# Optimization experiments

Hardware: AMD Instinct MI355X
Metric: run time of the kernel (lower is better)

## Reference

```python
import jax, jax.numpy as jnp
import numpy as np

B, CIN, H, W = 32, 64, 112, 112
COUT, KH, KW = 64, 3, 3
STRIDE = (1, 1)
PADDING = ((1, 1), (1, 1))
DILATION = (1, 1)


def setup_inputs() -> dict:
    key = jax.random.key(0)
    k1, k2, k3 = jax.random.split(key, 3)
    # quantized activations and weights, int8 value range [-128, 127]
    x_q = jax.random.randint(k1, (B, CIN, H, W), -128, 128, dtype=jnp.int32).astype(jnp.int8)
    w_q = jax.random.randint(k2, (COUT, CIN, KH, KW), -128, 128, dtype=jnp.int32).astype(jnp.int8)
    weight_scale = jnp.float32(0.02)   # per-tensor weight scale
    act_scale = jnp.float32(0.05)      # per-tensor activation scale
    bias = jax.random.normal(k3, (COUT,), dtype=jnp.float32)
    return {"x_q": x_q, "w_q": w_q, "weight_scale": weight_scale,
            "act_scale": act_scale, "bias": bias}


def reference(x_q, w_q, weight_scale, act_scale, bias):
    acc = jax.lax.conv_general_dilated(
        x_q.astype(jnp.int32), w_q.astype(jnp.int32),
        window_strides=STRIDE, padding=PADDING, rhs_dilation=DILATION,
        dimension_numbers=("NCHW", "OIHW", "NCHW"),
        preferred_element_type=jnp.int32)
    # fused dequant (per-tensor scales) + FP32 bias -> FP32 output [B, COUT, H, W]
    out = acc.astype(jnp.float32) * (act_scale * weight_scale) + bias[None, :, None, None]
    return out
```

## Files before the change

### kernel.cpp

```cpp
#include <hip/hip_runtime.h>
#include <stdint.h>

#define BATCH 32
#define CIN   64
#define HH    112
#define WW    112
#define COUT_ 64

typedef int v4i __attribute__((ext_vector_type(4)));

__global__ void wtrans_kernel(const int* __restrict__ wq, int8_t* __restrict__ wt) {
    int idx = blockIdx.x * 256 + threadIdx.x;
    int ci   = idx & 63;
    int khkw = (idx >> 6) % 9;
    int co   = idx / 576;
    wt[idx] = (int8_t)wq[co * 576 + ci * 9 + khkw];
}

__launch_bounds__(256, 2)
__global__ void conv_kernel(const int* __restrict__ x,
                            const int8_t* __restrict__ wt,
                            const float*  __restrict__ wscale,
                            const float*  __restrict__ ascale,
                            const float*  __restrict__ bias,
                            float*        __restrict__ out) {
    __shared__ int8_t xs[4 * 114 * 72];

    const int tid = threadIdx.x;
    const int bt  = blockIdx.x;
    const int b   = bt / 56;
    const int h0  = (bt % 56) * 2;

    #pragma unroll
    for (int it = 0; it < 7; ++it) {
        int job = tid + it * 256;
        int ci4 = job & 15;
        int cg  = (job >> 4) % 28;
        int row = job / 448;
        int hh  = h0 - 1 + row;
        v4i q0 = {0,0,0,0}, q1 = {0,0,0,0}, q2 = {0,0,0,0}, q3 = {0,0,0,0};
        if (hh >= 0 && hh < HH) {
            const v4i* gp = (const v4i*)
                (x + ((size_t)(b * CIN + ci4 * 4) * HH + hh) * WW + cg * 4);
            q0 = gp[0];
            q1 = gp[3136];
            q2 = gp[2 * 3136];
            q3 = gp[3 * 3136];
        }
        #pragma unroll
        for (int j = 0; j < 4; ++j) {
            uint32_t lo01 = __builtin_amdgcn_perm((uint32_t)q1[j], (uint32_t)q0[j], 0x0C0C0400u);
            uint32_t lo23 = __builtin_amdgcn_perm((uint32_t)q3[j], (uint32_t)q2[j], 0x04000C0Cu);
            int addr = (row * 114 + cg * 4 + 1 + j) * 72 + ci4 * 4;
            *(uint32_t*)&xs[addr] = lo01 | lo23;
        }
    }
    if (tid < 128) {
        int ci4 = tid & 15;
        int col = ((tid >> 4) & 1) ? 113 : 0;
        int row = tid >> 5;
        *(uint32_t*)&xs[(row * 114 + col) * 72 + ci4 * 4] = 0u;
    }
    __syncthreads();

    const int lane = tid & 63;
    const int wave = tid >> 6;
    const int ln15 = lane & 15;
    const int quad = lane >> 4;
    const int r    = wave >> 1;
    const int coh  = wave & 1;
    const int cobase = coh * 32;

    v4i acc[2][7];
    #pragma unroll
    for (int mt = 0; mt < 2; ++mt)
        #pragma unroll
        for (int nt = 0; nt < 7; ++nt)
            acc[mt][nt] = (v4i){0, 0, 0, 0};

    const long* w64a = (const long*)(wt + (size_t)(cobase + ln15) * 576);
    const long* w64b = (const long*)(wt + (size_t)(cobase + 16 + ln15) * 576);

    #pragma unroll
    for (int kc = 0; kc < 18; ++kc) {
        const int khkw = kc >> 1;
        const int kh   = khkw / 3;
        const int kw   = khkw % 3;
        const int half = kc & 1;
        long a0 = w64a[kc * 4 + quad];
        long a1 = w64b[kc * 4 + quad];
        const int rowb  = (kh + r) * 114;
        const int cioff = half * 32 + quad * 8;
        #pragma unroll
        for (int nt = 0; nt < 7; ++nt) {
            int col = nt * 16 + ln15 + kw;
            long bfrag = *(const long*)&xs[(rowb + col) * 72 + cioff];
            acc[0][nt] = __builtin_amdgcn_mfma_i32_16x16x32_i8(a0, bfrag, acc[0][nt], 0, 0, 0);
            acc[1][nt] = __builtin_amdgcn_mfma_i32_16x16x32_i8(a1, bfrag, acc[1][nt], 0, 0, 0);
        }
    }

    const float s = ascale[0] * wscale[0];
    const int h = h0 + r;
    #pragma unroll
    for (int mt = 0; mt < 2; ++mt) {
        #pragma unroll
        for (int reg = 0; reg < 4; ++reg) {
            int co = cobase + mt * 16 + quad * 4 + reg;
            float bv = bias[co];
            float* op = out + ((size_t)(b * COUT_ + co) * HH + h) * WW;
            #pragma unroll
            for (int nt = 0; nt < 7; ++nt) {
                int wp = nt * 16 + ln15;
                op[wp] = (float)acc[mt][nt][reg] * s + bv;
            }
        }
    }
}

extern "C" void kernel_launch(void* const* d_in, const int* in_sizes, int n_in,
                              void* d_out, int out_size, void* d_ws, size_t ws_size,
                              hipStream_t stream) {
    const int*    xq     = (const int*)d_in[0];
    const int*    wq     = (const int*)d_in[1];
    const float*  wscale = (const float*)d_in[2];
    const float*  ascale = (const float*)d_in[3];
    const float*  bias   = (const float*)d_in[4];
    int8_t* wt  = (int8_t*)d_ws;
    float*  out = (float*)d_out;

    wtrans_kernel<<<144, 256, 0, stream>>>(wq, wt);
    conv_kernel<<<BATCH * 56, 256, 0, stream>>>(xq, wt, wscale, ascale, bias, out);
}
```

Measured before the change: 213.1 us.

## Pre-transpose activations to swizzled int8 NHWC and use async LDS loads

Adds a separate pass that converts the int32 NCHW activations into a padded, XOR-swizzled int8 channel-last buffer in workspace. A new conv kernel then fills shared memory with direct global-to-LDS loads, keeps all nine weight taps in registers, and uses the wider 16x16x64 int8 MFMA. Each wave now handles 16 output channels across two rows, and occupancy is raised to 3 blocks per SM. The cost is an extra full pass over the input (read at int32, write at int8) and a workspace-size check, with the old kernel kept as a fallback.

```diff
diff --git a/kernel.cpp b/kernel.cpp
--- a/kernel.cpp
+++ b/kernel.cpp
@@ -8,6 +8,11 @@
 #define COUT_ 64
 
 typedef int v4i __attribute__((ext_vector_type(4)));
+
+#define WT_OFF   0
+#define ZP_OFF   36864
+#define XT_OFF   65536
+#define XT_NEED  (65536 + 26167296)
 
 __global__ void wtrans_kernel(const int* __restrict__ wq, int8_t* __restrict__ wt) {
     int idx = blockIdx.x * 256 + threadIdx.x;
@@ -15,6 +20,131 @@
     int khkw = (idx >> 6) % 9;
     int co   = idx / 576;
     wt[idx] = (int8_t)wq[co * 576 + ci * 9 + khkw];
+}
+
+__global__ void xtrans_kernel(const int* __restrict__ x, int8_t* __restrict__ ws) {
+    int8_t* __restrict__ xt = ws + XT_OFF;
+    const int bid = blockIdx.x;
+    const int tid = threadIdx.x;
+    if (bid < 6272) {
+        int idx  = bid * 256 + tid;
+        int ci4  = idx & 15;
+        int rest = idx >> 4;
+        int cg   = rest % 28;
+        int bh   = rest / 28;
+        int h    = bh % 112;
+        int b    = bh / 112;
+        const v4i* gp = (const v4i*)(x + ((b * CIN + ci4 * 4) * HH + h) * WW + cg * 4);
+        v4i q0 = gp[0];
+        v4i q1 = gp[3136];
+        v4i q2 = gp[2 * 3136];
+        v4i q3 = gp[3 * 3136];
+        int8_t* rowp = xt + (size_t)bh * 114 * 64;
+        #pragma unroll
+        for (int j = 0; j < 4; ++j) {
+            uint32_t lo01 = __builtin_amdgcn_perm((uint32_t)q1[j], (uint32_t)q0[j], 0x0C0C0400u);
+            uint32_t lo23 = __builtin_amdgcn_perm((uint32_t)q3[j], (uint32_t)q2[j], 0x04000C0Cu);
+            int col = cg * 4 + 1 + j;
+            int sd  = (((ci4 >> 2) ^ (col & 3)) << 2) | (ci4 & 3);
+            *(uint32_t*)&rowp[col * 64 + sd * 4] = lo01 | lo23;
+        }
+    } else if (bid < 6720) {
+        int idx  = (bid - 6272) * 256 + tid;
+        int d    = idx & 15;
+        int side = (idx >> 4) & 1;
+        int bh   = idx >> 5;
+        int col  = side ? 113 : 0;
+        *(uint32_t*)&xt[((size_t)bh * 114 + col) * 64 + d * 4] = 0u;
+    } else {
+        int idx = (bid - 6720) * 256 + tid;
+        if (idx < 1824) *(uint32_t*)&ws[ZP_OFF + idx * 4] = 0u;
+    }
+}
+
+__launch_bounds__(256, 3)
+__global__ void conv2_kernel(const int8_t* __restrict__ ws,
+                             const float*  __restrict__ wscale,
+                             const float*  __restrict__ ascale,
+                             const float*  __restrict__ bias,
+                             float*        __restrict__ out) {
+    __shared__ int8_t xs[4 * 114 * 64];
+
+    const int tid = threadIdx.x;
+    const int bt  = blockIdx.x;
+    const int b   = bt / 56;
+    const int h0  = (bt % 56) * 2;
+
+    const int8_t* __restrict__ xt = ws + XT_OFF;
+    const int8_t* __restrict__ zp = ws + ZP_OFF;
+    const int8_t* __restrict__ wt = ws + WT_OFF;
+
+    const int8_t* srow[4];
+    #pragma unroll
+    for (int r = 0; r < 4; ++r) {
+        int hh = h0 - 1 + r;
+        srow[r] = (hh >= 0 && hh < HH) ? xt + (size_t)(b * HH + hh) * 114 * 64 : zp;
+    }
+    #pragma unroll
+    for (int i = 0; i < 8; ++i) {
+        int idx = tid + i * 256;
+        if (idx < 1824) {
+            int row = idx / 456;
+            int rem = idx - row * 456;
+            __builtin_amdgcn_global_load_lds(
+                (const __attribute__((address_space(1))) int*)(srow[row] + rem * 16),
+                (__attribute__((address_space(3))) int*)(&xs[idx * 16]),
+                16, 0, 0);
+        }
+    }
+    __syncthreads();
+
+    const int lane = tid & 63;
+    const int wave = tid >> 6;
+    const int ln15 = lane & 15;
+    const int quad = lane >> 4;
+
+    const v4i* wrow = (const v4i*)(wt + (size_t)(wave * 16 + ln15) * 576);
+    v4i a[9];
+    #pragma unroll
+    for (int t = 0; t < 9; ++t) a[t] = wrow[t * 4 + quad];
+
+    v4i acc[2][7];
+    #pragma unroll
+    for (int r = 0; r < 2; ++r)
+        #pragma unroll
+        for (int nt = 0; nt < 7; ++nt)
+            acc[r][nt] = (v4i){0, 0, 0, 0};
+
+    #pragma unroll
+    for (int tap = 0; tap < 9; ++tap) {
+        const int kh = tap / 3;
+        const int kw = tap % 3;
+        const int swz = (quad ^ ((ln15 + kw) & 3)) << 4;
+        #pragma unroll
+        for (int r = 0; r < 2; ++r) {
+            const int8_t* bp = &xs[((kh + r) * 114 + ln15 + kw) * 64 + swz];
+            #pragma unroll
+            for (int nt = 0; nt < 7; ++nt) {
+                v4i bfrag = *(const v4i*)(bp + nt * 1024);
+                acc[r][nt] = __builtin_amdgcn_mfma_i32_16x16x64_i8(a[tap], bfrag, acc[r][nt], 0, 0, 0);
+            }
+        }
+    }
+
+    const float s = ascale[0] * wscale[0];
+    #pragma unroll
+    for (int r = 0; r < 2; ++r) {
+        const int h = h0 + r;
+        #pragma unroll
+        for (int reg = 0; reg < 4; ++reg) {
+            int co = wave * 16 + quad * 4 + reg;
+            float bv = bias[co];
+            float* op = out + ((size_t)(b * COUT_ + co) * HH + h) * WW;
+            #pragma unroll
+            for (int nt = 0; nt < 7; ++nt)
+                op[nt * 16 + ln15] = (float)acc[r][nt][reg] * s + bv;
+        }
+    }
 }
 
 __launch_bounds__(256, 2)
@@ -126,9 +256,14 @@
     const float*  wscale = (const float*)d_in[2];
     const float*  ascale = (const float*)d_in[3];
     const float*  bias   = (const float*)d_in[4];
-    int8_t* wt  = (int8_t*)d_ws;
+    int8_t* ws  = (int8_t*)d_ws;
     float*  out = (float*)d_out;
 
-    wtrans_kernel<<<144, 256, 0, stream>>>(wq, wt);
-    conv_kernel<<<BATCH * 56, 256, 0, stream>>>(xq, wt, wscale, ascale, bias, out);
-}
+    wtrans_kernel<<<144, 256, 0, stream>>>(wq, ws);
+    if (ws_size >= (size_t)XT_NEED) {
+        xtrans_kernel<<<6728, 256, 0, stream>>>(xq, ws);
+        conv2_kernel<<<BATCH * 56, 256, 0, stream>>>(ws, wscale, ascale, bias, out);
+    } else {
+        conv_kernel<<<BATCH * 56, 256, 0, stream>>>(xq, ws, wscale, ascale, bias, out);
+    }
+}
```

Result: slower. 222.8 us (+4.6%).

## Restructure int8 conv into persistent row-pipelined blocks with ring-buffered LDS

Applied to the files above, without the earlier changes.

Each block now handles 14 output rows of one image using an 8-row LDS ring buffer. It prefetches the next two input rows into registers while the MFMAs for the current pair run, which removes the per-block halo reload and overlaps global loads with compute. The kernel keeps the weights in registers for the whole block, switches to the 16x16x64 int8 MFMA, and applies an XOR swizzle to the LDS layout to avoid bank conflicts. The grid shrinks to 256 blocks, so only about one block per CU runs on the device, and register pressure rises.

```diff
diff --git a/kernel.cpp b/kernel.cpp
--- a/kernel.cpp
+++ b/kernel.cpp
@@ -9,6 +9,8 @@
 
 typedef int v4i __attribute__((ext_vector_type(4)));
 
+#define WT_OFF   0
+
 __global__ void wtrans_kernel(const int* __restrict__ wq, int8_t* __restrict__ wt) {
     int idx = blockIdx.x * 256 + threadIdx.x;
     int ci   = idx & 63;
@@ -18,101 +20,152 @@
 }
 
 __launch_bounds__(256, 2)
-__global__ void conv_kernel(const int* __restrict__ x,
-                            const int8_t* __restrict__ wt,
-                            const float*  __restrict__ wscale,
-                            const float*  __restrict__ ascale,
-                            const float*  __restrict__ bias,
-                            float*        __restrict__ out) {
-    __shared__ int8_t xs[4 * 114 * 72];
+__global__ void conv4_kernel(const int* __restrict__ x,
+                             const int8_t* __restrict__ wt,
+                             const float*  __restrict__ wscale,
+                             const float*  __restrict__ ascale,
+                             const float*  __restrict__ bias,
+                             float*        __restrict__ out) {
+    __shared__ int8_t xs[8 * 114 * 64];
 
     const int tid = threadIdx.x;
-    const int bt  = blockIdx.x;
-    const int b   = bt / 56;
-    const int h0  = (bt % 56) * 2;
-
-    #pragma unroll
-    for (int it = 0; it < 7; ++it) {
-        int job = tid + it * 256;
-        int ci4 = job & 15;
-        int cg  = (job >> 4) % 28;
-        int row = job / 448;
-        int hh  = h0 - 1 + row;
-        v4i q0 = {0,0,0,0}, q1 = {0,0,0,0}, q2 = {0,0,0,0}, q3 = {0,0,0,0};
-        if (hh >= 0 && hh < HH) {
-            const v4i* gp = (const v4i*)
-                (x + ((size_t)(b * CIN + ci4 * 4) * HH + hh) * WW + cg * 4);
-            q0 = gp[0];
-            q1 = gp[3136];
-            q2 = gp[2 * 3136];
-            q3 = gp[3 * 3136];
-        }
-        #pragma unroll
-        for (int j = 0; j < 4; ++j) {
-            uint32_t lo01 = __builtin_amdgcn_perm((uint32_t)q1[j], (uint32_t)q0[j], 0x0C0C0400u);
-            uint32_t lo23 = __builtin_amdgcn_perm((uint32_t)q3[j], (uint32_t)q2[j], 0x04000C0Cu);
-            int addr = (row * 114 + cg * 4 + 1 + j) * 72 + ci4 * 4;
-            *(uint32_t*)&xs[addr] = lo01 | lo23;
-        }
-    }
-    if (tid < 128) {
-        int ci4 = tid & 15;
-        int col = ((tid >> 4) & 1) ? 113 : 0;
-        int row = tid >> 5;
-        *(uint32_t*)&xs[(row * 114 + col) * 72 + ci4 * 4] = 0u;
-    }
-    __syncthreads();
+    const int b   = blockIdx.x >> 3;
+    const int hb  = (blockIdx.x & 7) * 14;
 
     const int lane = tid & 63;
     const int wave = tid >> 6;
     const int ln15 = lane & 15;
     const int quad = lane >> 4;
-    const int r    = wave >> 1;
-    const int coh  = wave & 1;
-    const int cobase = coh * 32;
 
-    v4i acc[2][7];
-    #pragma unroll
-    for (int mt = 0; mt < 2; ++mt)
-        #pragma unroll
-        for (int nt = 0; nt < 7; ++nt)
-            acc[mt][nt] = (v4i){0, 0, 0, 0};
-
-    const long* w64a = (const long*)(wt + (size_t)(cobase + ln15) * 576);
-    const long* w64b = (const long*)(wt + (size_t)(cobase + 16 + ln15) * 576);
-
-    #pragma unroll
-    for (int kc = 0; kc < 18; ++kc) {
-        const int khkw = kc >> 1;
-        const int kh   = khkw / 3;
-        const int kw   = khkw % 3;
-        const int half = kc & 1;
-        long a0 = w64a[kc * 4 + quad];
-        long a1 = w64b[kc * 4 + quad];
-        const int rowb  = (kh + r) * 114;
-        const int cioff = half * 32 + quad * 8;
-        #pragma unroll
-        for (int nt = 0; nt < 7; ++nt) {
-            int col = nt * 16 + ln15 + kw;
-            long bfrag = *(const long*)&xs[(rowb + col) * 72 + cioff];
-            acc[0][nt] = __builtin_amdgcn_mfma_i32_16x16x32_i8(a0, bfrag, acc[0][nt], 0, 0, 0);
-            acc[1][nt] = __builtin_amdgcn_mfma_i32_16x16x32_i8(a1, bfrag, acc[1][nt], 0, 0, 0);
-        }
+    {
+        int pr   = tid >> 5;
+        int side = (tid >> 4) & 1;
+        int d    = tid & 15;
+        *(uint32_t*)&xs[pr * 7296 + (side ? 113 : 0) * 64 + d * 4] = 0u;
     }
 
+    const v4i* wrow = (const v4i*)(wt + (size_t)(wave * 16 + ln15) * 576);
+    v4i a[9];
+    #pragma unroll
+    for (int t = 0; t < 9; ++t) a[t] = wrow[t * 4 + quad];
+
     const float s = ascale[0] * wscale[0];
-    const int h = h0 + r;
+    float bv[4];
     #pragma unroll
-    for (int mt = 0; mt < 2; ++mt) {
+    for (int reg = 0; reg < 4; ++reg) bv[reg] = bias[wave * 16 + quad * 4 + reg];
+
+    v4i q[16];
+    auto stage_load = [&](int hstart) {
         #pragma unroll
-        for (int reg = 0; reg < 4; ++reg) {
-            int co = cobase + mt * 16 + quad * 4 + reg;
-            float bv = bias[co];
-            float* op = out + ((size_t)(b * COUT_ + co) * HH + h) * WW;
+        for (int it = 0; it < 4; ++it) {
             #pragma unroll
-            for (int nt = 0; nt < 7; ++nt) {
-                int wp = nt * 16 + ln15;
-                op[wp] = (float)acc[mt][nt][reg] * s + bv;
+            for (int p = 0; p < 4; ++p) q[it * 4 + p] = (v4i){0, 0, 0, 0};
+            int job = tid + it * 256;
+            if (job < 896) {
+                int ci4  = job & 15;
+                int cg   = (job >> 4) % 28;
+                int row2 = job / 448;
+                int hh   = hstart + row2;
+                if (hh >= 0 && hh < HH) {
+                    const v4i* gp = (const v4i*)
+                        (x + ((size_t)(b * CIN + ci4 * 4) * HH + hh) * WW + cg * 4);
+                    q[it * 4 + 0] = gp[0];
+                    q[it * 4 + 1] = gp[3136];
+                    q[it * 4 + 2] = gp[2 * 3136];
+                    q[it * 4 + 3] = gp[3 * 3136];
+                }
+            }
+        }
+    };
+    auto stage_write = [&](int pb) {
+        #pragma unroll
+        for (int it = 0; it < 4; ++it) {
+            int job = tid + it * 256;
+            if (job < 896) {
+                int ci4  = job & 15;
+                int cg   = (job >> 4) % 28;
+                int row2 = job / 448;
+                int pr   = (pb + row2) & 7;
+                int8_t* rowp = &xs[pr * 7296];
+                #pragma unroll
+                for (int j = 0; j < 4; ++j) {
+                    uint32_t lo01 = __builtin_amdgcn_perm(
+                        (uint32_t)q[it * 4 + 1][j], (uint32_t)q[it * 4 + 0][j], 0x0C0C0400u);
+                    uint32_t lo23 = __builtin_amdgcn_perm(
+                        (uint32_t)q[it * 4 + 3][j], (uint32_t)q[it * 4 + 2][j], 0x04000C0Cu);
+                    int col = cg * 4 + 1 + j;
+                    int sd  = (((ci4 >> 2) ^ ((col >> 1) & 3)) << 2) | (ci4 & 3);
+                    *(uint32_t*)&rowp[col * 64 + sd * 4] = lo01 | lo23;
+                }
+            }
+        }
+    };
+
+    stage_load(hb - 1);
+    asm volatile("s_waitcnt vmcnt(0)" ::: "memory");
+    stage_write(0);
+    stage_load(hb + 1);
+    asm volatile("s_waitcnt vmcnt(0)" ::: "memory");
+    stage_write(2);
+    asm volatile("s_waitcnt lgkmcnt(0)" ::: "memory");
+    __builtin_amdgcn_s_barrier();
+    __builtin_amdgcn_sched_barrier(0);
+
+    #pragma unroll 1
+    for (int t = 0; t < 7; ++t) {
+        if (t < 6) {
+            stage_load(hb + 2 * t + 3);
+            __builtin_amdgcn_sched_barrier(0);
+        }
+
+        v4i acc[2][7];
+        #pragma unroll
+        for (int r = 0; r < 2; ++r)
+            #pragma unroll
+            for (int nt = 0; nt < 7; ++nt)
+                acc[r][nt] = (v4i){0, 0, 0, 0};
+
+        #pragma unroll
+        for (int rho = 0; rho < 4; ++rho) {
+            const int pr = (2 * t + rho) & 7;
+            #pragma unroll
+            for (int kw = 0; kw < 3; ++kw) {
+                const int m   = ln15 + kw;
+                const int swz = (quad ^ ((m >> 1) & 3)) << 4;
+                const int8_t* bp = &xs[pr * 7296 + m * 64 + swz];
+                #pragma unroll
+                for (int nt = 0; nt < 7; ++nt) {
+                    v4i bfrag = *(const v4i*)(bp + nt * 1024);
+                    if (rho <= 2)
+                        acc[0][nt] = __builtin_amdgcn_mfma_i32_16x16x64_i8(
+                            a[rho * 3 + kw], bfrag, acc[0][nt], 0, 0, 0);
+                    if (rho >= 1)
+                        acc[1][nt] = __builtin_amdgcn_mfma_i32_16x16x64_i8(
+                            a[(rho - 1) * 3 + kw], bfrag, acc[1][nt], 0, 0, 0);
+                }
+            }
+        }
+
+        __builtin_amdgcn_sched_barrier(0);
+        if (t < 6) {
+            asm volatile("s_waitcnt vmcnt(0)" ::: "memory");
+            stage_write((2 * t + 4) & 7);
+            asm volatile("s_waitcnt lgkmcnt(0)" ::: "memory");
+            __builtin_amdgcn_s_barrier();
+            __builtin_amdgcn_sched_barrier(0);
+        }
+
+        const int h0 = hb + 2 * t;
+        #pragma unroll
+        for (int r = 0; r < 2; ++r) {
+            const int h = h0 + r;
+            #pragma unroll
+            for (int reg = 0; reg < 4; ++reg) {
+                int co = wave * 16 + quad * 4 + reg;
+                float* op = out + ((size_t)(b * COUT_ + co) * HH + h) * WW;
+                #pragma unroll
+                for (int nt = 0; nt < 7; ++nt)
+                    op[nt * 16 + ln15] = (float)acc[r][nt][reg] * s + bv[reg];
             }
         }
     }
@@ -130,5 +183,5 @@
     float*  out = (float*)d_out;
 
     wtrans_kernel<<<144, 256, 0, stream>>>(wq, wt);
-    conv_kernel<<<BATCH * 56, 256, 0, stream>>>(xq, wt, wscale, ascale, bias, out);
+    conv4_kernel<<<256, 256, 0, stream>>>(xq, wt, wscale, ascale, bias, out);
 }
```

New measurement: 200.3 us. 1.06x faster.
